# Performance work log

Measured on AMD Instinct MI355X. Metric: run time of the kernel, lower is better.

Reference implementation:

```python
import jax, jax.numpy as jnp
import numpy as np

N, E, F, H, D, C = 50000, 800000, 128, 8, 16, 40


def setup_inputs() -> dict:
    key = jax.random.key(0)
    ks = jax.random.split(key, 12)
    s_in = 1.0 / np.sqrt(F)
    s_h = 1.0 / np.sqrt(H * D)
    return {
        "x": jax.random.normal(ks[0], (N, F), jnp.float32),
        "edge_index": jax.random.randint(ks[1], (2, E), 0, N, jnp.int64),
        "W1": jax.random.normal(ks[2], (F, H * D), jnp.float32) * s_in,
        "a_src1": jax.random.normal(ks[3], (H, D), jnp.float32) * s_h,
        "a_dst1": jax.random.normal(ks[4], (H, D), jnp.float32) * s_h,
        "b1": jnp.zeros((H * D,), jnp.float32),
        "W2": jax.random.normal(ks[5], (H * D, H * D), jnp.float32) * s_h,
        "a_src2": jax.random.normal(ks[6], (H, D), jnp.float32) * s_h,
        "a_dst2": jax.random.normal(ks[7], (H, D), jnp.float32) * s_h,
        "b2": jnp.zeros((H * D,), jnp.float32),
        "Wc": jax.random.normal(ks[8], (H * D, C), jnp.float32) * s_h,
        "bc": jnp.zeros((C,), jnp.float32),
    }


def _gat_layer(x, src, dst, W, a_src, a_dst, b):
    # x: [N, F_in]; src/dst: [E'] (self-loops already appended)
    n = x.shape[0]
    h, d = a_src.shape
    hx = (x @ W).reshape(n, h, d)                      # [N, H, D]
    al_src = jnp.einsum("nhd,hd->nh", hx, a_src)       # [N, H]
    al_dst = jnp.einsum("nhd,hd->nh", hx, a_dst)       # [N, H]
    e = jax.nn.leaky_relu(al_src[src] + al_dst[dst], 0.2)  # [E', H]
    # segment softmax over incoming edges of each destination node
    m = jax.ops.segment_max(e, dst, num_segments=n)    # [N, H]
    e = jnp.exp(e - m[dst])
    z = jax.ops.segment_sum(e, dst, num_segments=n)    # [N, H]
    alpha = e / z[dst]                                 # [E', H]
    out = jax.ops.segment_sum(alpha[:, :, None] * hx[src], dst, num_segments=n)
    return out.reshape(n, h * d) + b


def reference(x, edge_index, W1, a_src1, a_dst1, b1, W2, a_src2, a_dst2, b2, Wc, bc):
    n = x.shape[0]
    loops = jnp.arange(n, dtype=edge_index.dtype)
    src = jnp.concatenate([edge_index[0], loops])  # PyG GATConv adds self-loops
    dst = jnp.concatenate([edge_index[1], loops])
    h = _gat_layer(x, src, dst, W1, a_src1, a_dst1, b1)
    h = jax.nn.elu(h)  # ELU between layers (i < K-1); dropout=None -> no-op
    h = _gat_layer(h, src, dst, W2, a_src2, a_dst2, b2)
    return h @ Wc + bc  # [N, C] logits
```

## Files before the change

### kernel.cpp

```cpp
#include <hip/hip_runtime.h>
#include <hip/hip_bf16.h>


#define FDIM 128
#define HEADS 8
#define XS_PAD 136

__device__ __forceinline__ float leaky02(float x) {
    return fmaxf(x, 0.2f * x);
}

__device__ __forceinline__ unsigned pack2bf(float x, float y) {
    unsigned a = __float_as_uint(x), b = __float_as_uint(y);
    a += 0x7fffu + ((a >> 16) & 1u);
    b += 0x7fffu + ((b >> 16) & 1u);
    return (a >> 16) | (b & 0xffff0000u);
}


__global__ __launch_bounds__(256) void hist_rank_kernel(const int* __restrict__ ei,
                                                        int* __restrict__ deg,
                                                        int* __restrict__ rank,
                                                        int E) {
    int e = blockIdx.x * 256 + threadIdx.x;
    if (e >= E) return;
    rank[e] = atomicAdd(&deg[ei[E + e]], 1);
}

__global__ __launch_bounds__(256) void scan_partial(const int* __restrict__ deg,
                                                    int* __restrict__ partials,
                                                    int n) {
    __shared__ int red[256];
    int t = threadIdx.x;
    int base = blockIdx.x * 1024 + t * 4;
    int s = 0;
#pragma unroll
    for (int j = 0; j < 4; ++j) {
        int i = base + j;
        if (i < n) s += deg[i];
    }
    red[t] = s;
    __syncthreads();
    for (int off = 128; off > 0; off >>= 1) {
        if (t < off) red[t] += red[t + off];
        __syncthreads();
    }
    if (t == 0) partials[blockIdx.x] = red[0];
}

__global__ __launch_bounds__(64) void scan_offsets(int* __restrict__ partials,
                                                   int* __restrict__ row_start,
                                                   int nb, int n) {
    int lane = threadIdx.x;
    int carry = 0;
    for (int base = 0; base < nb; base += 64) {
        int idx = base + lane;
        int v = (idx < nb) ? partials[idx] : 0;
        int incl = v;
#pragma unroll
        for (int off = 1; off < 64; off <<= 1) {
            int t = __shfl_up(incl, off);
            if (lane >= off) incl += t;
        }
        if (idx < nb) partials[idx] = carry + incl - v;
        carry += __shfl(incl, 63);
    }
    if (lane == 0) row_start[n] = carry;
}

__global__ __launch_bounds__(256) void scan_final(const int* __restrict__ deg,
                                                  const int* __restrict__ partials,
                                                  int* __restrict__ row_start,
                                                  int n) {
    __shared__ int sbuf[256];
    int t = threadIdx.x;
    int base = blockIdx.x * 1024 + t * 4;
    int v[4];
#pragma unroll
    for (int j = 0; j < 4; ++j) v[j] = (base + j < n) ? deg[base + j] : 0;
    int tsum = v[0] + v[1] + v[2] + v[3];
    sbuf[t] = tsum;
    __syncthreads();
    for (int off = 1; off < 256; off <<= 1) {
        int tmp = (t >= off) ? sbuf[t - off] : 0;
        __syncthreads();
        sbuf[t] += tmp;
        __syncthreads();
    }
    int toff = partials[blockIdx.x] + sbuf[t] - tsum;
    int run = 0;
#pragma unroll
    for (int j = 0; j < 4; ++j) {
        int i = base + j;
        if (i < n) row_start[i] = toff + run;
        run += v[j];
    }
}


template <bool SCATTER>
__global__ __launch_bounds__(256, 8) void gemm128(const float* __restrict__ A,
                                                  const float* __restrict__ W,
                                                  const float* __restrict__ asrc,
                                                  const float* __restrict__ adst,
                                                  float* __restrict__ als,
                                                  float* __restrict__ ald,
                                                  unsigned* __restrict__ outb,
                                                  int n,
                                                  const int* __restrict__ ei,
                                                  const int* __restrict__ rank,
                                                  const int* __restrict__ row_start,
                                                  int* __restrict__ csr_src,
                                                  int E, int ng, int grid) {
    int tid = threadIdx.x;
    int gb;
    if (SCATTER) {
        int bid = blockIdx.x;
        int t0 = (int)((long long)bid * ng / grid);
        int t1 = (int)((long long)(bid + 1) * ng / grid);
        if (t1 == t0) {
            int sb = bid - t0;
#pragma unroll
            for (int j = 0; j < 4; ++j) {
                int e = sb * 1024 + j * 256 + tid;
                if (e < E) {
                    int s = ei[e];
                    int d = ei[E + e];
                    csr_src[row_start[d] + rank[e]] = s;
                }
            }
            return;
        }
        gb = t0;
    } else {
        gb = blockIdx.x;
    }

    {
        int q = ng >> 3, r8 = ng & 7;
        int xcd = gb & 7, loc = gb >> 3;
        int base = (xcd < r8) ? xcd * (q + 1) : r8 * (q + 1) + (xcd - r8) * q;
        gb = base + loc;
    }
    int row0 = (gb >> 2) * 128;
    int col0 = (gb & 3) * 32;

    __shared__ float smem[32 * XS_PAD + 32 * 36];
    float (*xs)[XS_PAD] = (float(*)[XS_PAD])smem;
    float (*ws)[36] = (float(*)[36])(smem + 32 * XS_PAD);

    int lane = tid & 63;
    int wave = tid >> 6;
    int lane2 = lane * 2;
    int wc = wave * 8;

    float acc[2][8];
#pragma unroll
    for (int i = 0; i < 2; ++i)
#pragma unroll
        for (int j = 0; j < 8; ++j) acc[i][j] = 0.f;

    for (int c = 0; c < 4; ++c) {
        int kc = c * 32;
        if (c) __syncthreads();
#pragma unroll
        for (int it = 0; it < 4; ++it) {
            int idx = it * 256 + tid;
            int r = idx >> 3;
            int kg = (idx & 7) * 4;
            float4 v = make_float4(0.f, 0.f, 0.f, 0.f);
            if (row0 + r < n)
                v = *(const float4*)&A[(size_t)(row0 + r) * FDIM + kc + kg];
            int col = r ^ kg;
            xs[kg + 0][col] = v.x;
            xs[kg + 1][col] = v.y;
            xs[kg + 2][col] = v.z;
            xs[kg + 3][col] = v.w;
        }
        {
            int kk = tid >> 3;
            int cc = (tid & 7) * 4;
            *(float4*)&ws[kk][cc] =
                *(const float4*)&W[(size_t)(kc + kk) * FDIM + col0 + cc];
        }
        __syncthreads();
#pragma unroll
        for (int k = 0; k < 32; ++k) {
            int s = ((k >> 2) & 7) << 2;
            float2 av2 = *(const float2*)&xs[k][lane2 ^ s];
            float4 w0 = *(const float4*)&ws[k][wc];
            float4 w1 = *(const float4*)&ws[k][wc + 4];
            float av[2] = {av2.x, av2.y};
            float wv[8] = {w0.x, w0.y, w0.z, w0.w, w1.x, w1.y, w1.z, w1.w};
#pragma unroll
            for (int i = 0; i < 2; ++i)
#pragma unroll
                for (int j = 0; j < 8; ++j)
                    acc[i][j] += av[i] * wv[j];
        }
    }

#pragma unroll
    for (int i = 0; i < 2; ++i) {
        int row = row0 + lane2 + i;
        if (row < n) {
            uint4 pk;
            pk.x = pack2bf(acc[i][0], acc[i][1]);
            pk.y = pack2bf(acc[i][2], acc[i][3]);
            pk.z = pack2bf(acc[i][4], acc[i][5]);
            pk.w = pack2bf(acc[i][6], acc[i][7]);
            *(uint4*)&outb[(size_t)row * 64 + (col0 + wc) / 2] = pk;
        }
    }

    float ps[2], pd[2];
#pragma unroll
    for (int i = 0; i < 2; ++i) {
        float s0 = 0.f, s1 = 0.f;
#pragma unroll
        for (int c = 0; c < 8; ++c) {
            s0 += acc[i][c] * asrc[col0 + wc + c];
            s1 += acc[i][c] * adst[col0 + wc + c];
        }
        ps[i] = s0;
        pd[i] = s1;
    }
    __syncthreads();
    float* sal = smem;
    {
        float* mine = sal + tid * 4;
        mine[0] = ps[0];
        mine[1] = ps[1];
        mine[2] = pd[0];
        mine[3] = pd[1];
    }
    __syncthreads();
    if ((wave & 1) == 0) {
        const float* part = sal + ((wave ^ 1) * 64 + lane) * 4;
        int h = (col0 + wc) >> 4;
#pragma unroll
        for (int i = 0; i < 2; ++i) {
            int row = row0 + lane2 + i;
            if (row < n) {
                als[row * HEADS + h] = ps[i] + part[i];
                ald[row * HEADS + h] = pd[i] + part[2 + i];
            }
        }
    }
}


__global__ __launch_bounds__(256, 8) void gemm_cls(const float* __restrict__ A,
                                                   const float* __restrict__ W,
                                                   const float* __restrict__ bias,
                                                   float* __restrict__ out,
                                                   int n) {
    __shared__ float xs[32][XS_PAD];
    __shared__ float ws[32][48];
    int tid = threadIdx.x;
    int row0 = blockIdx.x * 128;
    int lane = tid & 63;
    int wave = tid >> 6;
    int lane2 = lane * 2;

    int wc = wave * 10;

    float acc[2][10];
#pragma unroll
    for (int i = 0; i < 2; ++i)
#pragma unroll
        for (int j = 0; j < 10; ++j) acc[i][j] = 0.f;

    for (int kc = 0; kc < 128; kc += 32) {
        if (kc) __syncthreads();
#pragma unroll
        for (int it = 0; it < 4; ++it) {
            int idx = it * 256 + tid;
            int r = idx >> 3, kg = (idx & 7) * 4;
            float4 v = make_float4(0.f, 0.f, 0.f, 0.f);
            if (row0 + r < n)
                v = *(const float4*)&A[(size_t)(row0 + r) * FDIM + kc + kg];
            int col = r ^ kg;
            xs[kg + 0][col] = v.x;
            xs[kg + 1][col] = v.y;
            xs[kg + 2][col] = v.z;
            xs[kg + 3][col] = v.w;
        }
#pragma unroll
        for (int it = 0; it < 6; ++it) {
            int idx = it * 256 + tid;
            int kk = idx / 48, c = idx - kk * 48;
            ws[kk][c] = (c < 40) ? W[(size_t)(kc + kk) * 40 + c] : 0.f;
        }
        __syncthreads();
#pragma unroll
        for (int k = 0; k < 32; ++k) {
            int s = ((k >> 2) & 7) << 2;
            float2 av2 = *(const float2*)&xs[k][lane2 ^ s];
            float av[2] = {av2.x, av2.y};
#pragma unroll
            for (int j = 0; j < 10; ++j) {
                float w = ws[k][wc + j];
                acc[0][j] += av[0] * w;
                acc[1][j] += av[1] * w;
            }
        }
    }

#pragma unroll
    for (int i = 0; i < 2; ++i) {
        int row = row0 + lane2 + i;
        if (row < n) {
#pragma unroll
            for (int j = 0; j < 10; ++j)
                out[(size_t)row * 40 + wc + j] = acc[i][j] + bias[wc + j];
        }
    }
}


template <bool DOELU>
__global__ __launch_bounds__(256) void gat_aggregate(const unsigned* __restrict__ hxb,
                                                     const float* __restrict__ als,
                                                     const float* __restrict__ ald,
                                                     const int* __restrict__ row_start,
                                                     const int* __restrict__ csr_src,
                                                     const float* __restrict__ bias,
                                                     float* __restrict__ out,
                                                     int n) {
    int wid = threadIdx.x >> 6;
    int lane = threadIdx.x & 63;
    int node = blockIdx.x * 4 + wid;
    if (node >= n) return;

    int rs = row_start[node];
    int deg = row_start[node + 1] - rs;

    int h = lane & 7;
    int hc = lane >> 3;
    float ald_h = ald[node * HEADS + h];

    float acc0 = 0.f, acc1 = 0.f, z = 0.f;
    int total = deg + 1;
    int i0 = 0;
    for (; i0 + 8 <= total; i0 += 8) {
        int ii = i0 + (lane >> 3);
        int srcv = (ii < deg) ? csr_src[rs + ii] : node;
        float w = __expf(leaky02(als[srcv * HEADS + h] + ald_h));
#pragma unroll
        for (int e = 0; e < 8; ++e) {
            int s    = __shfl(srcv, e * 8);
            float we = __shfl(w, e * 8 + hc);
            unsigned v = hxb[(size_t)s * 64 + lane];
            z += we;
            acc0 += we * __uint_as_float(v << 16);
            acc1 += we * __uint_as_float(v & 0xffff0000u);
        }
    }
    {
        int ii = i0 + (lane >> 3);
        int srcv = (ii < deg) ? csr_src[rs + ii] : node;
        float w = (ii < total) ? __expf(leaky02(als[srcv * HEADS + h] + ald_h)) : 0.f;
        int rem = total - i0;
        for (int e = 0; e < rem; ++e) {
            int s    = __shfl(srcv, e * 8);
            float we = __shfl(w, e * 8 + hc);
            unsigned v = hxb[(size_t)s * 64 + lane];
            z += we;
            acc0 += we * __uint_as_float(v << 16);
            acc1 += we * __uint_as_float(v & 0xffff0000u);
        }
    }

    float2 bv = *(const float2*)&bias[2 * lane];
    float o0 = acc0 / z + bv.x;
    float o1 = acc1 / z + bv.y;
    if (DOELU) {
        o0 = o0 > 0.f ? o0 : (__expf(o0) - 1.f);
        o1 = o1 > 0.f ? o1 : (__expf(o1) - 1.f);
    }
    *(float2*)&out[(size_t)node * FDIM + 2 * lane] = make_float2(o0, o1);
}


extern "C" void kernel_launch(void* const* d_in, const int* in_sizes, int n_in,
                              void* d_out, int out_size, void* d_ws, size_t ws_size,
                              hipStream_t stream) {
    const float* x      = (const float*)d_in[0];
    const int*   ei     = (const int*)d_in[1];
    const float* W1     = (const float*)d_in[2];
    const float* a_src1 = (const float*)d_in[3];
    const float* a_dst1 = (const float*)d_in[4];
    const float* b1     = (const float*)d_in[5];
    const float* W2     = (const float*)d_in[6];
    const float* a_src2 = (const float*)d_in[7];
    const float* a_dst2 = (const float*)d_in[8];
    const float* b2     = (const float*)d_in[9];
    const float* Wc     = (const float*)d_in[10];
    const float* bc     = (const float*)d_in[11];
    float* out = (float*)d_out;

    const int N = in_sizes[0] / FDIM;
    const int E = in_sizes[1] / 2;
    const int NB = (N + 1023) / 1024;

    unsigned* hxb = (unsigned*)d_ws;
    float* hbuf = (float*)(hxb + (size_t)N * 64);
    float* als  = hbuf + (size_t)N * FDIM;
    float* ald  = als + (size_t)N * HEADS;
    int* deg       = (int*)(ald + (size_t)N * HEADS);
    int* row_start = deg + N;
    int* partials  = row_start + ((N + 8) & ~3);
    int* rank      = partials + ((NB + 4) & ~3);
    int* csr_src   = rank + E;

    hipMemsetAsync(deg, 0, (size_t)N * sizeof(int), stream);
    hist_rank_kernel<<<(E + 255) / 256, 256, 0, stream>>>(ei, deg, rank, E);
    scan_partial<<<NB, 256, 0, stream>>>(deg, partials, N);
    scan_offsets<<<1, 64, 0, stream>>>(partials, row_start, NB, N);
    scan_final<<<NB, 256, 0, stream>>>(deg, partials, row_start, N);

    const int ng = ((N + 127) / 128) * 4;
    const int ns = (E + 1023) / 1024;
    const int grid1 = ng + ns;
    const int agg_grid = (N + 3) / 4;
    const int cls_grid = (N + 127) / 128;

    gemm128<true><<<grid1, 256, 0, stream>>>(x, W1, a_src1, a_dst1,
                                             als, ald, hxb, N,
                                             ei, rank, row_start, csr_src, E,
                                             ng, grid1);
    gat_aggregate<true><<<agg_grid, 256, 0, stream>>>(hxb, als, ald, row_start,
                                                      csr_src, b1, hbuf, N);
    gemm128<false><<<ng, 256, 0, stream>>>(hbuf, W2, a_src2, a_dst2,
                                           als, ald, hxb, N,
                                           nullptr, nullptr, nullptr,
                                           nullptr, 0, ng, ng);
    gat_aggregate<false><<<agg_grid, 256, 0, stream>>>(hxb, als, ald, row_start,
                                                       csr_src, b2, hbuf, N);
    gemm_cls<<<cls_grid, 256, 0, stream>>>(hbuf, Wc, bc, out, N);
}
```

Measured before the change: 240.6 us.

## Replace FP32 SIMT GEMMs with split-bf16 MFMA and hi/lo activation storage

Swaps the two 128x128 feature GEMMs from scalar FP32 FMA tiles to bf16 MFMA instructions, using a hi/lo bf16 split with three MFMAs per tile to keep near-FP32 accuracy. A new prep kernel, merged with the histogram step, splits x and the weights into hi/lo bf16 and pre-swizzles the weights into MFMA fragment order. The aggregate kernel now writes its output as hi/lo bf16 pairs, and the classifier GEMM reconstructs FP32 from them. This is meant to cut the FP32 ALU cost of the GEMMs, in exchange for an extra pass that converts x and for more MFMA work per tile.

```diff
diff --git a/kernel.cpp b/kernel.cpp
--- a/kernel.cpp
+++ b/kernel.cpp
@@ -4,7 +4,9 @@
 
 #define FDIM 128
 #define HEADS 8
-#define XS_PAD 136
+
+typedef short bf16x8 __attribute__((ext_vector_type(8)));
+typedef float f32x4 __attribute__((ext_vector_type(4)));
 
 __device__ __forceinline__ float leaky02(float x) {
     return fmaxf(x, 0.2f * x);
@@ -17,15 +19,83 @@
     return (a >> 16) | (b & 0xffff0000u);
 }
 
-
-__global__ __launch_bounds__(256) void hist_rank_kernel(const int* __restrict__ ei,
-                                                        int* __restrict__ deg,
-                                                        int* __restrict__ rank,
-                                                        int E) {
-    int e = blockIdx.x * 256 + threadIdx.x;
-    if (e >= E) return;
-    rank[e] = atomicAdd(&deg[ei[E + e]], 1);
-}
+__device__ __forceinline__ void split2(float x, unsigned short& hi, unsigned short& lo) {
+    unsigned bits = __float_as_uint(x);
+    unsigned h = bits + 0x7fffu + ((bits >> 16) & 1u);
+    hi = (unsigned short)(h >> 16);
+    float hf = __uint_as_float(h & 0xffff0000u);
+    float r = x - hf;
+    unsigned rb = __float_as_uint(r);
+    unsigned l2 = rb + 0x7fffu + ((rb >> 16) & 1u);
+    lo = (unsigned short)(l2 >> 16);
+}
+
+
+__global__ __launch_bounds__(256) void prep_kernel(const int* __restrict__ ei,
+                                                   int* __restrict__ deg,
+                                                   int* __restrict__ rank,
+                                                   int E,
+                                                   const float* __restrict__ x,
+                                                   unsigned short* __restrict__ x_hi,
+                                                   unsigned short* __restrict__ x_lo,
+                                                   int nel,
+                                                   const float* __restrict__ W1,
+                                                   const float* __restrict__ W2,
+                                                   unsigned short* __restrict__ w1_hi,
+                                                   unsigned short* __restrict__ w1_lo,
+                                                   unsigned short* __restrict__ w2_hi,
+                                                   unsigned short* __restrict__ w2_lo,
+                                                   int histB, int xB) {
+    int b = blockIdx.x, t = threadIdx.x;
+    if (b < histB) {
+        int e = b * 256 + t;
+        if (e < E) rank[e] = atomicAdd(&deg[ei[E + e]], 1);
+        return;
+    }
+    b -= histB;
+    if (b < xB) {
+        int i0 = (b * 256 + t) * 8;
+        if (i0 < nel) {
+            float4 v0 = *(const float4*)&x[i0];
+            float4 v1 = *(const float4*)&x[i0 + 4];
+            float vv[8] = {v0.x, v0.y, v0.z, v0.w, v1.x, v1.y, v1.z, v1.w};
+            unsigned short h[8], l[8];
+#pragma unroll
+            for (int j = 0; j < 8; ++j) split2(vv[j], h[j], l[j]);
+            uint4 hh, ll;
+            hh.x = h[0] | ((unsigned)h[1] << 16);
+            hh.y = h[2] | ((unsigned)h[3] << 16);
+            hh.z = h[4] | ((unsigned)h[5] << 16);
+            hh.w = h[6] | ((unsigned)h[7] << 16);
+            ll.x = l[0] | ((unsigned)l[1] << 16);
+            ll.y = l[2] | ((unsigned)l[3] << 16);
+            ll.z = l[4] | ((unsigned)l[5] << 16);
+            ll.w = l[6] | ((unsigned)l[7] << 16);
+            *(uint4*)&x_hi[i0] = hh;
+            *(uint4*)&x_lo[i0] = ll;
+        }
+        return;
+    }
+    b -= xB;
+    const float* W = (b < 16) ? W1 : W2;
+    unsigned short* whi = (b < 16) ? w1_hi : w2_hi;
+    unsigned short* wlo = (b < 16) ? w1_lo : w2_lo;
+    int idx = (b & 15) * 256 + t;
+    int k = idx >> 5;
+    int c0 = (idx & 31) * 4;
+#pragma unroll
+    for (int i = 0; i < 4; ++i) {
+        int c = c0 + i;
+        float v = W[k * FDIM + c];
+        unsigned short h, l;
+        split2(v, h, l);
+        int dest = ((k >> 5) * 8 + (c >> 4)) * 512 +
+                   ((c & 15) + (((k >> 3) & 3) << 4)) * 8 + (k & 7);
+        whi[dest] = h;
+        wlo[dest] = l;
+    }
+}
+
 
 __global__ __launch_bounds__(256) void scan_partial(const int* __restrict__ deg,
                                                     int* __restrict__ partials,
@@ -99,19 +169,21 @@
 
 
 template <bool SCATTER>
-__global__ __launch_bounds__(256, 8) void gemm128(const float* __restrict__ A,
-                                                  const float* __restrict__ W,
-                                                  const float* __restrict__ asrc,
-                                                  const float* __restrict__ adst,
-                                                  float* __restrict__ als,
-                                                  float* __restrict__ ald,
-                                                  unsigned* __restrict__ outb,
-                                                  int n,
-                                                  const int* __restrict__ ei,
-                                                  const int* __restrict__ rank,
-                                                  const int* __restrict__ row_start,
-                                                  int* __restrict__ csr_src,
-                                                  int E, int ng, int grid) {
+__global__ __launch_bounds__(256, 4) void gemm_mfma(const unsigned short* __restrict__ a_hi,
+                                                    const unsigned short* __restrict__ a_lo,
+                                                    const unsigned short* __restrict__ w_hi,
+                                                    const unsigned short* __restrict__ w_lo,
+                                                    const float* __restrict__ asrc,
+                                                    const float* __restrict__ adst,
+                                                    float* __restrict__ als,
+                                                    float* __restrict__ ald,
+                                                    unsigned* __restrict__ hxb,
+                                                    int n,
+                                                    const int* __restrict__ ei,
+                                                    const int* __restrict__ rank,
+                                                    const int* __restrict__ row_start,
+                                                    int* __restrict__ csr_src,
+                                                    int E, int ng, int grid) {
     int tid = threadIdx.x;
     int gb;
     if (SCATTER) {
@@ -136,133 +208,98 @@
         gb = blockIdx.x;
     }
 
-    {
-        int q = ng >> 3, r8 = ng & 7;
-        int xcd = gb & 7, loc = gb >> 3;
-        int base = (xcd < r8) ? xcd * (q + 1) : r8 * (q + 1) + (xcd - r8) * q;
-        gb = base + loc;
-    }
-    int row0 = (gb >> 2) * 128;
-    int col0 = (gb & 3) * 32;
-
-    __shared__ float smem[32 * XS_PAD + 32 * 36];
-    float (*xs)[XS_PAD] = (float(*)[XS_PAD])smem;
-    float (*ws)[36] = (float(*)[36])(smem + 32 * XS_PAD);
-
     int lane = tid & 63;
     int wave = tid >> 6;
-    int lane2 = lane * 2;
-    int wc = wave * 8;
-
-    float acc[2][8];
-#pragma unroll
-    for (int i = 0; i < 2; ++i)
-#pragma unroll
-        for (int j = 0; j < 8; ++j) acc[i][j] = 0.f;
-
-    for (int c = 0; c < 4; ++c) {
-        int kc = c * 32;
-        if (c) __syncthreads();
-#pragma unroll
-        for (int it = 0; it < 4; ++it) {
-            int idx = it * 256 + tid;
-            int r = idx >> 3;
-            int kg = (idx & 7) * 4;
-            float4 v = make_float4(0.f, 0.f, 0.f, 0.f);
-            if (row0 + r < n)
-                v = *(const float4*)&A[(size_t)(row0 + r) * FDIM + kc + kg];
-            int col = r ^ kg;
-            xs[kg + 0][col] = v.x;
-            xs[kg + 1][col] = v.y;
-            xs[kg + 2][col] = v.z;
-            xs[kg + 3][col] = v.w;
-        }
-        {
-            int kk = tid >> 3;
-            int cc = (tid & 7) * 4;
-            *(float4*)&ws[kk][cc] =
-                *(const float4*)&W[(size_t)(kc + kk) * FDIM + col0 + cc];
-        }
-        __syncthreads();
-#pragma unroll
-        for (int k = 0; k < 32; ++k) {
-            int s = ((k >> 2) & 7) << 2;
-            float2 av2 = *(const float2*)&xs[k][lane2 ^ s];
-            float4 w0 = *(const float4*)&ws[k][wc];
-            float4 w1 = *(const float4*)&ws[k][wc + 4];
-            float av[2] = {av2.x, av2.y};
-            float wv[8] = {w0.x, w0.y, w0.z, w0.w, w1.x, w1.y, w1.z, w1.w};
-#pragma unroll
-            for (int i = 0; i < 2; ++i)
-#pragma unroll
-                for (int j = 0; j < 8; ++j)
-                    acc[i][j] += av[i] * wv[j];
-        }
-    }
-
-#pragma unroll
-    for (int i = 0; i < 2; ++i) {
-        int row = row0 + lane2 + i;
-        if (row < n) {
-            uint4 pk;
-            pk.x = pack2bf(acc[i][0], acc[i][1]);
-            pk.y = pack2bf(acc[i][2], acc[i][3]);
-            pk.z = pack2bf(acc[i][4], acc[i][5]);
-            pk.w = pack2bf(acc[i][6], acc[i][7]);
-            *(uint4*)&outb[(size_t)row * 64 + (col0 + wc) / 2] = pk;
-        }
-    }
-
-    float ps[2], pd[2];
-#pragma unroll
-    for (int i = 0; i < 2; ++i) {
-        float s0 = 0.f, s1 = 0.f;
-#pragma unroll
-        for (int c = 0; c < 8; ++c) {
-            s0 += acc[i][c] * asrc[col0 + wc + c];
-            s1 += acc[i][c] * adst[col0 + wc + c];
-        }
-        ps[i] = s0;
-        pd[i] = s1;
-    }
-    __syncthreads();
-    float* sal = smem;
-    {
-        float* mine = sal + tid * 4;
-        mine[0] = ps[0];
-        mine[1] = ps[1];
-        mine[2] = pd[0];
-        mine[3] = pd[1];
-    }
-    __syncthreads();
-    if ((wave & 1) == 0) {
-        const float* part = sal + ((wave ^ 1) * 64 + lane) * 4;
-        int h = (col0 + wc) >> 4;
-#pragma unroll
-        for (int i = 0; i < 2; ++i) {
-            int row = row0 + lane2 + i;
-            if (row < n) {
-                als[row * HEADS + h] = ps[i] + part[i];
-                ald[row * HEADS + h] = pd[i] + part[2 + i];
+    int l15 = lane & 15;
+    int lg = lane >> 4;
+    int row0 = gb * 32;
+
+    f32x4 acc[2][2];
+#pragma unroll
+    for (int fr = 0; fr < 2; ++fr)
+#pragma unroll
+        for (int fc = 0; fc < 2; ++fc)
+#pragma unroll
+            for (int r = 0; r < 4; ++r) acc[fr][fc][r] = 0.f;
+
+#pragma unroll
+    for (int kc = 0; kc < 4; ++kc) {
+        bf16x8 Ah[2], Al[2], Bh[2], Bl[2];
+#pragma unroll
+        for (int fr = 0; fr < 2; ++fr) {
+            int r = row0 + fr * 16 + l15;
+            if (r > n - 1) r = n - 1;
+            size_t off = (size_t)r * FDIM + kc * 32 + lg * 8;
+            Ah[fr] = *(const bf16x8*)(a_hi + off);
+            Al[fr] = *(const bf16x8*)(a_lo + off);
+        }
+#pragma unroll
+        for (int fc = 0; fc < 2; ++fc) {
+            int FC = wave * 2 + fc;
+            size_t off = (size_t)(kc * 8 + FC) * 512 + lane * 8;
+            Bh[fc] = *(const bf16x8*)(w_hi + off);
+            Bl[fc] = *(const bf16x8*)(w_lo + off);
+        }
+#pragma unroll
+        for (int fr = 0; fr < 2; ++fr)
+#pragma unroll
+            for (int fc = 0; fc < 2; ++fc) {
+                acc[fr][fc] = __builtin_amdgcn_mfma_f32_16x16x32_bf16(
+                    Al[fr], Bh[fc], acc[fr][fc], 0, 0, 0);
+                acc[fr][fc] = __builtin_amdgcn_mfma_f32_16x16x32_bf16(
+                    Ah[fr], Bl[fc], acc[fr][fc], 0, 0, 0);
+                acc[fr][fc] = __builtin_amdgcn_mfma_f32_16x16x32_bf16(
+                    Ah[fr], Bh[fc], acc[fr][fc], 0, 0, 0);
             }
-        }
-    }
-}
-
-
-__global__ __launch_bounds__(256, 8) void gemm_cls(const float* __restrict__ A,
+    }
+
+#pragma unroll
+    for (int fr = 0; fr < 2; ++fr)
+#pragma unroll
+        for (int fc = 0; fc < 2; ++fc) {
+            int CB = wave * 32 + fc * 16;
+            int col = CB + l15;
+            float as_ = asrc[col];
+            float ad_ = adst[col];
+#pragma unroll
+            for (int reg = 0; reg < 4; ++reg) {
+                int row = row0 + fr * 16 + lg * 4 + reg;
+                float v = acc[fr][fc][reg];
+                float vn = __shfl_xor(v, 1);
+                if ((lane & 1) == 0 && row < n)
+                    hxb[(size_t)row * 64 + (col >> 1)] = pack2bf(v, vn);
+                float ps = v * as_;
+                float pd = v * ad_;
+                ps += __shfl_xor(ps, 1);
+                pd += __shfl_xor(pd, 1);
+                ps += __shfl_xor(ps, 2);
+                pd += __shfl_xor(pd, 2);
+                ps += __shfl_xor(ps, 4);
+                pd += __shfl_xor(pd, 4);
+                ps += __shfl_xor(ps, 8);
+                pd += __shfl_xor(pd, 8);
+                if (l15 == 0 && row < n) {
+                    als[row * HEADS + (CB >> 4)] = ps;
+                    ald[row * HEADS + (CB >> 4)] = pd;
+                }
+            }
+        }
+}
+
+
+__global__ __launch_bounds__(256, 8) void gemm_cls(const unsigned* __restrict__ h_hi,
+                                                   const unsigned* __restrict__ h_lo,
                                                    const float* __restrict__ W,
                                                    const float* __restrict__ bias,
                                                    float* __restrict__ out,
                                                    int n) {
-    __shared__ float xs[32][XS_PAD];
+    __shared__ float xs[32][136];
     __shared__ float ws[32][48];
     int tid = threadIdx.x;
     int row0 = blockIdx.x * 128;
     int lane = tid & 63;
     int wave = tid >> 6;
     int lane2 = lane * 2;
-
     int wc = wave * 10;
 
     float acc[2][10];
@@ -278,8 +315,14 @@
             int idx = it * 256 + tid;
             int r = idx >> 3, kg = (idx & 7) * 4;
             float4 v = make_float4(0.f, 0.f, 0.f, 0.f);
-            if (row0 + r < n)
-                v = *(const float4*)&A[(size_t)(row0 + r) * FDIM + kc + kg];
+            if (row0 + r < n) {
+                uint2 hh = *(const uint2*)&h_hi[(size_t)(row0 + r) * 64 + (kc + kg) / 2];
+                uint2 ll = *(const uint2*)&h_lo[(size_t)(row0 + r) * 64 + (kc + kg) / 2];
+                v.x = __uint_as_float(hh.x << 16) + __uint_as_float(ll.x << 16);
+                v.y = __uint_as_float(hh.x & 0xffff0000u) + __uint_as_float(ll.x & 0xffff0000u);
+                v.z = __uint_as_float(hh.y << 16) + __uint_as_float(ll.y << 16);
+                v.w = __uint_as_float(hh.y & 0xffff0000u) + __uint_as_float(ll.y & 0xffff0000u);
+            }
             int col = r ^ kg;
             xs[kg + 0][col] = v.x;
             xs[kg + 1][col] = v.y;
@@ -326,7 +369,8 @@
                                                      const int* __restrict__ row_start,
                                                      const int* __restrict__ csr_src,
                                                      const float* __restrict__ bias,
-                                                     float* __restrict__ out,
+                                                     unsigned* __restrict__ h_hi,
+                                                     unsigned* __restrict__ h_lo,
                                                      int n) {
     int wid = threadIdx.x >> 6;
     int lane = threadIdx.x & 63;
@@ -379,7 +423,11 @@
         o0 = o0 > 0.f ? o0 : (__expf(o0) - 1.f);
         o1 = o1 > 0.f ? o1 : (__expf(o1) - 1.f);
     }
-    *(float2*)&out[(size_t)node * FDIM + 2 * lane] = make_float2(o0, o1);
+    unsigned short h0, l0, h1, l1;
+    split2(o0, h0, l0);
+    split2(o1, h1, l1);
+    h_hi[(size_t)node * 64 + lane] = (unsigned)h0 | ((unsigned)h1 << 16);
+    h_lo[(size_t)node * 64 + lane] = (unsigned)l0 | ((unsigned)l1 << 16);
 }
 
 
@@ -403,40 +451,53 @@
     const int N = in_sizes[0] / FDIM;
     const int E = in_sizes[1] / 2;
     const int NB = (N + 1023) / 1024;
+    const int nel = N * FDIM;
 
     unsigned* hxb = (unsigned*)d_ws;
-    float* hbuf = (float*)(hxb + (size_t)N * 64);
-    float* als  = hbuf + (size_t)N * FDIM;
+    unsigned* xh_u = hxb + (size_t)N * 64;
+    unsigned* xl_u = xh_u + (size_t)N * 64;
+    float* als  = (float*)(xl_u + (size_t)N * 64);
     float* ald  = als + (size_t)N * HEADS;
-    int* deg       = (int*)(ald + (size_t)N * HEADS);
+    unsigned short* w1_hi = (unsigned short*)(ald + (size_t)N * HEADS);
+    unsigned short* w1_lo = w1_hi + 16384;
+    unsigned short* w2_hi = w1_lo + 16384;
+    unsigned short* w2_lo = w2_hi + 16384;
+    int* deg       = (int*)(w2_lo + 16384);
     int* row_start = deg + N;
     int* partials  = row_start + ((N + 8) & ~3);
     int* rank      = partials + ((NB + 4) & ~3);
     int* csr_src   = rank + E;
 
+    unsigned short* x_hi = (unsigned short*)xh_u;
+    unsigned short* x_lo = (unsigned short*)xl_u;
+
     hipMemsetAsync(deg, 0, (size_t)N * sizeof(int), stream);
-    hist_rank_kernel<<<(E + 255) / 256, 256, 0, stream>>>(ei, deg, rank, E);
+    const int histB = (E + 255) / 256;
+    const int xB = (nel + 2047) / 2048;
+    prep_kernel<<<histB + xB + 32, 256, 0, stream>>>(
+        ei, deg, rank, E, x, x_hi, x_lo, nel,
+        W1, W2, w1_hi, w1_lo, w2_hi, w2_lo, histB, xB);
     scan_partial<<<NB, 256, 0, stream>>>(deg, partials, N);
     scan_offsets<<<1, 64, 0, stream>>>(partials, row_start, NB, N);
     scan_final<<<NB, 256, 0, stream>>>(deg, partials, row_start, N);
 
-    const int ng = ((N + 127) / 128) * 4;
+    const int ng = (N + 31) / 32;
     const int ns = (E + 1023) / 1024;
     const int grid1 = ng + ns;
     const int agg_grid = (N + 3) / 4;
     const int cls_grid = (N + 127) / 128;
 
-    gemm128<true><<<grid1, 256, 0, stream>>>(x, W1, a_src1, a_dst1,
-                                             als, ald, hxb, N,
-                                             ei, rank, row_start, csr_src, E,
-                                             ng, grid1);
+    gemm_mfma<true><<<grid1, 256, 0, stream>>>(x_hi, x_lo, w1_hi, w1_lo,
+                                               a_src1, a_dst1, als, ald, hxb, N,
+                                               ei, rank, row_start, csr_src,
+                                               E, ng, grid1);
     gat_aggregate<true><<<agg_grid, 256, 0, stream>>>(hxb, als, ald, row_start,
-                                                      csr_src, b1, hbuf, N);
-    gemm128<false><<<ng, 256, 0, stream>>>(hbuf, W2, a_src2, a_dst2,
-                                           als, ald, hxb, N,
-                                           nullptr, nullptr, nullptr,
-                                           nullptr, 0, ng, ng);
+                                                      csr_src, b1, xh_u, xl_u, N);
+    gemm_mfma<false><<<ng, 256, 0, stream>>>(x_hi, x_lo, w2_hi, w2_lo,
+                                             a_src2, a_dst2, als, ald, hxb, N,
+                                             nullptr, nullptr, nullptr, nullptr,
+                                             0, ng, ng);
     gat_aggregate<false><<<agg_grid, 256, 0, stream>>>(hxb, als, ald, row_start,
-                                                       csr_src, b2, hbuf, N);
-    gemm_cls<<<cls_grid, 256, 0, stream>>>(hbuf, Wc, bc, out, N);
-}
+                                                       csr_src, b2, xh_u, xl_u, N);
+    gemm_cls<<<cls_grid, 256, 0, stream>>>(xh_u, xl_u, Wc, bc, out, N);
+}
```

After: 235.7 us. -2.0%, faster.
